# Optimization experiments

Hardware: AMD Instinct MI355X
Metric: run time of the kernel (lower is better)

Reference implementation:

```python
import jax, jax.numpy as jnp
import numpy as np

B = 4096        # batch_size
D = 128         # embedding dim
TEMP = 0.5      # temperature
EPS = 1e-8      # torch CosineSimilarity eps


def _mask_indices(batch_size):
    """Static flat indices replicating torch boolean-mask (row-major) gather."""
    n = 2 * batch_size
    pos = np.eye(n, n, k=batch_size, dtype=np.float64)
    tril = np.tril(np.ones((n, n), dtype=np.float64))
    neg = (1.0 - tril - pos).astype(bool)
    pos_idx = np.flatnonzero(pos.astype(bool).ravel())
    neg_idx = np.flatnonzero(neg.ravel())
    return jnp.asarray(pos_idx), jnp.asarray(neg_idx)

_POS_IDX, _NEG_IDX = _mask_indices(B)


def setup_inputs() -> dict:
    key = jax.random.key(0)
    k1, k2 = jax.random.split(key)
    zis = jax.random.normal(k1, (B, D), dtype=jnp.float32)
    zjs = jax.random.normal(k2, (B, D), dtype=jnp.float32)
    return {"zis": zis, "zjs": zjs}


def reference(zis, zjs):
    # representations = cat([zjs, zis])  -> [2B, D]
    reps = jnp.concatenate([zjs, zis], axis=0)
    # cosine similarity matrix via normalize + GEMM (same math as broadcasted CosineSimilarity)
    norm = jnp.sqrt(jnp.sum(reps * reps, axis=-1, keepdims=True))
    nreps = reps / jnp.maximum(norm, EPS)
    sim = nreps @ nreps.T                      # [2B, 2B]
    flat = sim.reshape(-1)
    positives = flat[_POS_IDX].reshape(B, -1)  # [B, 1]
    negatives = flat[_NEG_IDX].reshape(B, -1)  # [B, 2B-2]
    logits = jnp.concatenate([positives, negatives], axis=1) / TEMP  # [B, 2B-1]
    # CrossEntropy with labels all zero, reduction='sum'
    logp = jax.nn.log_softmax(logits, axis=-1)
    loss = -jnp.sum(logp[:, 0])
    return loss / B
```

## Files before the change

### kernel.cpp

```cpp
#include <hip/hip_runtime.h>
#include <hip/hip_bf16.h>
#include <math.h>

#define B_  4096u
#define N_  8192
#define D_  128
#define M_  8190u
#define SB_ 25159680u
#define NT2_ 1056

#define AS1 __attribute__((address_space(1)))
#define AS3 __attribute__((address_space(3)))

typedef __attribute__((ext_vector_type(8))) int   i32x8;
typedef __attribute__((ext_vector_type(4))) int   i32x4;
typedef __attribute__((ext_vector_type(4))) float f32x4;

static __device__ __forceinline__ unsigned rowS(unsigned i) {
  if (i <= B_) return i * (2u * B_ - 2u) - (i * (i - 1u)) / 2u;
  unsigned d = i - B_;
  return SB_ + d * (B_ - 1u) - (d * (d - 1u)) / 2u;
}
static __device__ __forceinline__ int tile0(int m) {
  return 32 * m - (m * m - 2 * m + (m & 1)) / 4;
}
template <int CTRL>
static __device__ __forceinline__ float dpp_add(float x) {
  union { float f; int i; } u, r;
  u.f = x;
  r.i = __builtin_amdgcn_mov_dpp(u.i, CTRL, 0xF, 0xF, 0);
  return x + r.f;
}
static __device__ __forceinline__ float rsum16(float x) {
  x = dpp_add<0x121>(x);
  x = dpp_add<0x122>(x);
  x = dpp_add<0x124>(x);
  x = dpp_add<0x128>(x);
  return x;
}

__global__ __launch_bounds__(256) void nt_norm(
    const float* __restrict__ zis, const float* __restrict__ zjs,
    unsigned* __restrict__ nb8, unsigned* __restrict__ Trow,
    unsigned* __restrict__ zbase) {
  const int t   = threadIdx.x;
  const int row = blockIdx.x * 8 + (t >> 5);
  const int c   = t & 31;
  const float* src = (row < (int)B_) ? (zjs + (size_t)row * D_)
                                     : (zis + (size_t)(row - (int)B_) * D_);
  float4 v = *(const float4*)(src + c * 4);
  float s = v.x * v.x + v.y * v.y + v.z * v.z + v.w * v.w;
  #pragma unroll
  for (int m = 16; m >= 1; m >>= 1) s += __shfl_xor(s, m, 32);
  float rn = 1.0f / fmaxf(sqrtf(s), 1e-8f);
  int p = __builtin_amdgcn_cvt_pk_fp8_f32(v.x * rn, v.y * rn, 0, false);
  p     = __builtin_amdgcn_cvt_pk_fp8_f32(v.z * rn, v.w * rn, p, true);
  nb8[(size_t)row * 32 + c] = (unsigned)p;

  if (t < 8) {
    unsigned i   = (unsigned)(blockIdx.x * 8 + t);
    unsigned S   = rowS(i);
    unsigned rlo = S / M_;
    unsigned Sh  = (rlo + 1u) * M_;
    unsigned jt  = Sh - S + i + 1u;
    Trow[i] = jt + ((i < B_ && jt > i + B_) ? 1u : 0u);
  }
  if (blockIdx.x == 0) {
    for (int r = t; r < 4128; r += 256) zbase[r] = 0u;
  }
}

__global__ __launch_bounds__(512, 4) void nt_gemm(
    const char* __restrict__ nb, const unsigned* __restrict__ Trow,
    float2* __restrict__ part, float* __restrict__ posl) {
  const int tb = ((int)blockIdx.x & 7) * 132 + ((int)blockIdx.x >> 3);
  int bi2 = (int)(2.0f * (32.0f - sqrtf(fmaxf(0.f, 1024.0f - (float)tb))));
  if (bi2 > 63) bi2 = 63;
  while (bi2 > 0 && tb < tile0(bi2)) --bi2;
  while (tb >= tile0(bi2 + 1)) ++bi2;
  const int jlo = bi2 >> 1;
  const int bj2 = jlo + (tb - tile0(bi2));

  __shared__ char Asm[128 * 128];
  __shared__ char Bsm[256 * 128];
  __shared__ float2 red2[4][128];

  const int t    = threadIdx.x;
  const int lane = t & 63, wave = t >> 6;
  const int li   = lane & 15, hi = lane >> 4;
  const int wr   = wave >> 2, wc = wave & 3;
  const int i0   = bi2 * 128, j0 = bj2 * 256;

  const char* gA = nb + (size_t)i0 * 128;
  const char* gB = nb + (size_t)j0 * 128;

  #pragma unroll
  for (int it = 0; it < 2; ++it) {
    int e = it * 512 + t, r = e >> 3, sl = e & 7, sg = sl ^ (r & 7);
    __builtin_amdgcn_global_load_lds(
        (const AS1 void*)(gA + (size_t)r * 128 + sg * 16),
        (AS3 void*)(Asm + e * 16), 16, 0, 0);
  }
  #pragma unroll
  for (int it = 0; it < 4; ++it) {
    int e = it * 512 + t, r = e >> 3, sl = e & 7, sg = sl ^ (r & 7);
    __builtin_amdgcn_global_load_lds(
        (const AS1 void*)(gB + (size_t)r * 128 + sg * 16),
        (AS3 void*)(Bsm + e * 16), 16, 0, 0);
  }

  f32x4 acc[4][4];
  #pragma unroll
  for (int m = 0; m < 4; ++m)
    #pragma unroll
    for (int n = 0; n < 4; ++n) acc[m][n] = (f32x4){0.f, 0.f, 0.f, 0.f};

  asm volatile("s_waitcnt vmcnt(0)" ::: "memory");
  __builtin_amdgcn_s_barrier();
  __builtin_amdgcn_sched_barrier(0);

  i32x8 af[4];
  #pragma unroll
  for (int m = 0; m < 4; ++m) {
    const int R = wr * 64 + m * 16 + li, rb = R & 7;
    i32x4 lo = *(const i32x4*)(Asm + (size_t)R * 128 + (((hi << 1)    ) ^ rb) * 16);
    i32x4 hv = *(const i32x4*)(Asm + (size_t)R * 128 + (((hi << 1) | 1) ^ rb) * 16);
    af[m][0] = lo[0]; af[m][1] = lo[1]; af[m][2] = lo[2]; af[m][3] = lo[3];
    af[m][4] = hv[0]; af[m][5] = hv[1]; af[m][6] = hv[2]; af[m][7] = hv[3];
  }

  __builtin_amdgcn_s_setprio(1);
  #pragma unroll
  for (int n = 0; n < 4; ++n) {
    const int R = wc * 64 + n * 16 + li, rb = R & 7;
    i32x4 lo = *(const i32x4*)(Bsm + (size_t)R * 128 + (((hi << 1)    ) ^ rb) * 16);
    i32x4 hv = *(const i32x4*)(Bsm + (size_t)R * 128 + (((hi << 1) | 1) ^ rb) * 16);
    i32x8 bfr;
    bfr[0] = lo[0]; bfr[1] = lo[1]; bfr[2] = lo[2]; bfr[3] = lo[3];
    bfr[4] = hv[0]; bfr[5] = hv[1]; bfr[6] = hv[2]; bfr[7] = hv[3];
    #pragma unroll
    for (int m = 0; m < 4; ++m)
      acc[m][n] = __builtin_amdgcn_mfma_scale_f32_16x16x128_f8f6f4(
          af[m], bfr, acc[m][n], 0, 0,
          0, 127,
          0, 127);
  }
  __builtin_amdgcn_s_setprio(0);

  const bool isdiag = (bj2 == jlo);
  const bool ispost = (bj2 == jlo + 16);
  const bool special = isdiag | ispost;
  const unsigned jw0 = (unsigned)(j0 + wc * 64);

  #pragma unroll
  for (int m = 0; m < 4; ++m) {
    const uint4 T4 = *(const uint4*)(Trow + i0 + wr * 64 + m * 16 + hi * 4);
    const unsigned Ts[4] = {T4.x, T4.y, T4.z, T4.w};
    #pragma unroll
    for (int rg = 0; rg < 4; ++rg) {
      const unsigned i = (unsigned)(i0 + wr * 64 + m * 16 + hi * 4 + rg);
      const unsigned T = Ts[rg];
      float r0, r1;
      if (special) {
        float s0 = 0.f, s1 = 0.f;
        #pragma unroll
        for (int n = 0; n < 4; ++n) {
          const unsigned j = jw0 + n * 16 + (unsigned)li;
          const bool ip = ispost && (j == i + B_);
          if (ip) posl[i] = 2.0f * acc[m][n][rg];
          if ((j > i) && !ip) {
            float e = __expf(2.0f * acc[m][n][rg]);
            if (j < T) s0 += e; else s1 += e;
          }
        }
        r0 = rsum16(s0); r1 = rsum16(s1);
      } else if ((T > jw0) && (T < jw0 + 64u)) {
        float s0 = 0.f, s1 = 0.f;
        #pragma unroll
        for (int n = 0; n < 4; ++n) {
          const unsigned j = jw0 + n * 16 + (unsigned)li;
          float e = __expf(2.0f * acc[m][n][rg]);
          if (j < T) s0 += e; else s1 += e;
        }
        r0 = rsum16(s0); r1 = rsum16(s1);
      } else {
        float s = 0.f;
        #pragma unroll
        for (int n = 0; n < 4; ++n) s += __expf(2.0f * acc[m][n][rg]);
        s = rsum16(s);
        const bool lo = (T > jw0);
        r0 = lo ? s : 0.f;
        r1 = lo ? 0.f : s;
      }
      if (li == 0)
        red2[wc][wr * 64 + m * 16 + hi * 4 + rg] = make_float2(r0, r1);
    }
  }
  __syncthreads();

  if (t < 128) {
    float2 s = make_float2(0.f, 0.f);
    #pragma unroll
    for (int w = 0; w < 4; ++w) {
      float2 v = red2[w][t];
      s.x += v.x; s.y += v.y;
    }
    part[(size_t)tb * 128 + t] = s;
  }
}

__global__ __launch_bounds__(256) void nt_rowfin(
    const float2* __restrict__ part, const float* __restrict__ posl,
    float* __restrict__ E, unsigned* __restrict__ counter,
    float* __restrict__ out) {
  __shared__ float2 xch[128];
  __shared__ float Epan[132];
  __shared__ int lastflag;
  __shared__ double red[256];
  const int bi2 = (int)blockIdx.x;
  const int t = threadIdx.x;
  const int lrow = t & 127, sh = t >> 7;
  const int base = tile0(bi2);
  const int cnt  = 32 - (bi2 >> 1);
  const unsigned i0     = (unsigned)(bi2 * 128);
  const unsigned rstart = rowS(i0) / M_;
  const unsigned rspan  = rowS(i0 + 127u) / M_ + 1u - rstart + 1u;

  if (t < 132) Epan[t] = 0.f;

  float2 s = make_float2(0.f, 0.f);
  for (int c = sh; c < cnt; c += 2) {
    float2 v = part[(size_t)(base + c) * 128 + lrow];
    s.x += v.x; s.y += v.y;
  }
  if (sh == 1) xch[lrow] = s;
  __syncthreads();
  if (sh == 0) {
    float2 v = xch[lrow];
    s.x += v.x; s.y += v.y;
    const unsigned i   = i0 + (unsigned)lrow;
    const unsigned rlo = rowS(i) / M_;
    atomicAdd(&Epan[rlo - rstart],      s.x);
    atomicAdd(&Epan[rlo - rstart + 1u], s.y);
  }
  __syncthreads();
  if (t < (int)rspan) {
    float v = Epan[t];
    if (v != 0.f) atomicAdd(&E[rstart + (unsigned)t], v);
  }
  __threadfence();
  __syncthreads();
  if (t == 0) lastflag = (atomicAdd(counter, 1u) == 63u) ? 1 : 0;
  __syncthreads();
  if (!lastflag) return;

  __threadfence();
  double acc = 0.0;
  for (int r = t; r < (int)B_; r += 256) {
    float ev = __hip_atomic_load(&E[r], __ATOMIC_RELAXED,
                                 __HIP_MEMORY_SCOPE_AGENT);
    float pl = posl[r];
    acc += (double)(logf(__expf(pl) + ev) - pl);
  }
  red[t] = acc;
  __syncthreads();
  for (int m = 128; m > 0; m >>= 1) {
    if (t < m) red[t] += red[t + m];
    __syncthreads();
  }
  if (t == 0) out[0] = (float)(red[0] / (double)B_);
}

extern "C" void kernel_launch(void* const* d_in, const int* in_sizes, int n_in,
                              void* d_out, int out_size, void* d_ws, size_t ws_size,
                              hipStream_t stream) {
  const float* zis = (const float*)d_in[0];
  const float* zjs = (const float*)d_in[1];
  float* out = (float*)d_out;

  char* ws = (char*)d_ws;
  char*     nb      = ws;
  unsigned* Trow    = (unsigned*)(ws + 1048576);
  float*    posl    = (float*)(ws + 1081344);
  float2*   part    = (float2*)(ws + 1097728);
  float*    E       = (float*)(ws + 2179072);
  unsigned* counter = (unsigned*)(ws + 2195520);
  unsigned* zb      = (unsigned*)E;

  nt_norm  <<<dim3(N_ / 8), 256, 0, stream>>>(zis, zjs, (unsigned*)nb, Trow, zb);
  nt_gemm  <<<dim3(NT2_),   512, 0, stream>>>(nb, Trow, part, posl);
  nt_rowfin<<<dim3(64),     256, 0, stream>>>(part, posl, E, counter, out);
}
```

Measured before the change: 45.99 us.

## Fuse normalization and FP8 packing into the GEMM kernel, drop norm launch

Removes the separate normalization kernel. Each GEMM block now loads its 384 fp32 rows directly, computes norms with wave shuffles, converts to fp8 and writes the swizzled tiles into LDS. The per-row threshold T is computed inline instead of read from a precomputed buffer. This saves a kernel launch and the round trip through the intermediate fp8 buffer, but every block repeats normalization of the rows it uses (about 1056 blocks × 384 rows) and reads fp32 data, which is four times the bytes of the fp8 copy.

```diff
diff --git a/kernel.cpp b/kernel.cpp
--- a/kernel.cpp
+++ b/kernel.cpp
@@ -24,6 +24,12 @@
 static __device__ __forceinline__ int tile0(int m) {
   return 32 * m - (m * m - 2 * m + (m & 1)) / 4;
 }
+static __device__ __forceinline__ unsigned rowT(unsigned i) {
+  unsigned S = rowS(i);
+  unsigned T = (S / M_ + 1u) * M_ - S + i + 1u;
+  T += ((i < B_) && (T > i + B_)) ? 1u : 0u;
+  return T;
+}
 template <int CTRL>
 static __device__ __forceinline__ float dpp_add(float x) {
   union { float f; int i; } u, r;
@@ -39,40 +45,14 @@
   return x;
 }
 
-__global__ __launch_bounds__(256) void nt_norm(
+__global__ __launch_bounds__(512, 4) void nt_gemm(
     const float* __restrict__ zis, const float* __restrict__ zjs,
-    unsigned* __restrict__ nb8, unsigned* __restrict__ Trow,
-    unsigned* __restrict__ zbase) {
-  const int t   = threadIdx.x;
-  const int row = blockIdx.x * 8 + (t >> 5);
-  const int c   = t & 31;
-  const float* src = (row < (int)B_) ? (zjs + (size_t)row * D_)
-                                     : (zis + (size_t)(row - (int)B_) * D_);
-  float4 v = *(const float4*)(src + c * 4);
-  float s = v.x * v.x + v.y * v.y + v.z * v.z + v.w * v.w;
-  #pragma unroll
-  for (int m = 16; m >= 1; m >>= 1) s += __shfl_xor(s, m, 32);
-  float rn = 1.0f / fmaxf(sqrtf(s), 1e-8f);
-  int p = __builtin_amdgcn_cvt_pk_fp8_f32(v.x * rn, v.y * rn, 0, false);
-  p     = __builtin_amdgcn_cvt_pk_fp8_f32(v.z * rn, v.w * rn, p, true);
-  nb8[(size_t)row * 32 + c] = (unsigned)p;
-
-  if (t < 8) {
-    unsigned i   = (unsigned)(blockIdx.x * 8 + t);
-    unsigned S   = rowS(i);
-    unsigned rlo = S / M_;
-    unsigned Sh  = (rlo + 1u) * M_;
-    unsigned jt  = Sh - S + i + 1u;
-    Trow[i] = jt + ((i < B_ && jt > i + B_) ? 1u : 0u);
-  }
+    float2* __restrict__ part, float* __restrict__ posl,
+    unsigned* __restrict__ zb) {
   if (blockIdx.x == 0) {
-    for (int r = t; r < 4128; r += 256) zbase[r] = 0u;
-  }
-}
-
-__global__ __launch_bounds__(512, 4) void nt_gemm(
-    const char* __restrict__ nb, const unsigned* __restrict__ Trow,
-    float2* __restrict__ part, float* __restrict__ posl) {
+    for (int r = threadIdx.x; r < 4128; r += 512) zb[r] = 0u;
+  }
+
   const int tb = ((int)blockIdx.x & 7) * 132 + ((int)blockIdx.x >> 3);
   int bi2 = (int)(2.0f * (32.0f - sqrtf(fmaxf(0.f, 1024.0f - (float)tb))));
   if (bi2 > 63) bi2 = 63;
@@ -91,33 +71,33 @@
   const int wr   = wave >> 2, wc = wave & 3;
   const int i0   = bi2 * 128, j0 = bj2 * 256;
 
-  const char* gA = nb + (size_t)i0 * 128;
-  const char* gB = nb + (size_t)j0 * 128;
-
-  #pragma unroll
-  for (int it = 0; it < 2; ++it) {
-    int e = it * 512 + t, r = e >> 3, sl = e & 7, sg = sl ^ (r & 7);
-    __builtin_amdgcn_global_load_lds(
-        (const AS1 void*)(gA + (size_t)r * 128 + sg * 16),
-        (AS3 void*)(Asm + e * 16), 16, 0, 0);
-  }
-  #pragma unroll
-  for (int it = 0; it < 4; ++it) {
-    int e = it * 512 + t, r = e >> 3, sl = e & 7, sg = sl ^ (r & 7);
-    __builtin_amdgcn_global_load_lds(
-        (const AS1 void*)(gB + (size_t)r * 128 + sg * 16),
-        (AS3 void*)(Bsm + e * 16), 16, 0, 0);
-  }
+  #pragma unroll
+  for (int half = 0; half < 2; ++half) {
+    for (int rr = wave + half * 8; rr < 384; rr += 16) {
+      const bool isA = (rr < 128);
+      const int  rl  = isA ? rr : rr - 128;
+      const int  R   = isA ? (i0 + rl) : (j0 + rl);
+      const float* src = (R < (int)B_) ? (zjs + (size_t)R * D_)
+                                       : (zis + (size_t)(R - (int)B_) * D_);
+      float2 v = *(const float2*)(src + lane * 2);
+      float s = v.x * v.x + v.y * v.y;
+      #pragma unroll
+      for (int m = 32; m >= 1; m >>= 1) s += __shfl_xor(s, m, 64);
+      float rn = 1.0f / fmaxf(sqrtf(s), 1e-8f);
+      int p = __builtin_amdgcn_cvt_pk_fp8_f32(v.x * rn, v.y * rn, 0, false);
+      char* dst = isA ? Asm : Bsm;
+      *(unsigned short*)(dst + rl * 128 +
+                         (((lane >> 3) ^ (rl & 7)) * 16) + ((lane & 7) * 2)) =
+          (unsigned short)(p & 0xffff);
+    }
+  }
+  __syncthreads();
 
   f32x4 acc[4][4];
   #pragma unroll
   for (int m = 0; m < 4; ++m)
     #pragma unroll
     for (int n = 0; n < 4; ++n) acc[m][n] = (f32x4){0.f, 0.f, 0.f, 0.f};
-
-  asm volatile("s_waitcnt vmcnt(0)" ::: "memory");
-  __builtin_amdgcn_s_barrier();
-  __builtin_amdgcn_sched_barrier(0);
 
   i32x8 af[4];
   #pragma unroll
@@ -154,12 +134,10 @@
 
   #pragma unroll
   for (int m = 0; m < 4; ++m) {
-    const uint4 T4 = *(const uint4*)(Trow + i0 + wr * 64 + m * 16 + hi * 4);
-    const unsigned Ts[4] = {T4.x, T4.y, T4.z, T4.w};
     #pragma unroll
     for (int rg = 0; rg < 4; ++rg) {
       const unsigned i = (unsigned)(i0 + wr * 64 + m * 16 + hi * 4 + rg);
-      const unsigned T = Ts[rg];
+      const unsigned T = rowT(i);
       float r0, r1;
       if (special) {
         float s0 = 0.f, s1 = 0.f;
@@ -279,15 +257,12 @@
   float* out = (float*)d_out;
 
   char* ws = (char*)d_ws;
-  char*     nb      = ws;
-  unsigned* Trow    = (unsigned*)(ws + 1048576);
-  float*    posl    = (float*)(ws + 1081344);
-  float2*   part    = (float2*)(ws + 1097728);
-  float*    E       = (float*)(ws + 2179072);
-  unsigned* counter = (unsigned*)(ws + 2195520);
+  float*    posl    = (float*)ws;
+  float2*   part    = (float2*)(ws + 16384);
+  float*    E       = (float*)(ws + 16384 + 1081344);
+  unsigned* counter = (unsigned*)(ws + 16384 + 1081344 + 16448);
   unsigned* zb      = (unsigned*)E;
 
-  nt_norm  <<<dim3(N_ / 8), 256, 0, stream>>>(zis, zjs, (unsigned*)nb, Trow, zb);
-  nt_gemm  <<<dim3(NT2_),   512, 0, stream>>>(nb, Trow, part, posl);
-  nt_rowfin<<<dim3(64),     256, 0, stream>>>(part, posl, E, counter, out);
-}
+  nt_gemm  <<<dim3(NT2_), 512, 0, stream>>>(zis, zjs, part, posl, zb);
+  nt_rowfin<<<dim3(64),   256, 0, stream>>>(part, posl, E, counter, out);
+}
```

Measured after the change: 104.7 us. 128% more time.
